# Performance work log

Measured on AMD Instinct MI355X. Metric: run time of the kernel, lower is better.

Reference implementation:

```python
import jax, jax.numpy as jnp
import numpy as np

NUM_GROUPS = 32
EPS = 1e-6


def group_norm(x, gamma, beta):
    # x: (b, c, h, w) -> normalize within 32 groups over (c/g, h, w)
    b, c, h, w = x.shape
    g = NUM_GROUPS
    xg = x.reshape(b, g, c // g, h, w)
    mean = xg.mean(axis=(2, 3, 4), keepdims=True)
    var = xg.var(axis=(2, 3, 4), keepdims=True)
    xg = (xg - mean) * jax.lax.rsqrt(var + EPS)
    xn = xg.reshape(b, c, h, w)
    return xn * gamma[None, :, None, None] + beta[None, :, None, None]


def setup_inputs() -> dict:
    key = jax.random.key(0)
    ks = jax.random.split(key, 4)
    b, c, h, w = 4, 512, 64, 64
    x = jax.random.normal(ks[0], (b, c, h, w), dtype=jnp.float32)
    gamma = jnp.ones((c,), dtype=jnp.float32)
    beta = jnp.zeros((c,), dtype=jnp.float32)
    w_qkv = jax.random.normal(ks[1], (3 * c, c), dtype=jnp.float32) * (1.0 / np.sqrt(c))
    b_qkv = jnp.zeros((3 * c,), dtype=jnp.float32)
    # NOTE: original init zeroes proj weight; use small random weights so the
    # attention path contributes to output/gradients in the baseline.
    w_proj = jax.random.normal(ks[2], (c, c), dtype=jnp.float32) * 0.02
    b_proj = jnp.zeros((c,), dtype=jnp.float32)
    return {"x": x, "gamma": gamma, "beta": beta, "w_qkv": w_qkv,
            "b_qkv": b_qkv, "w_proj": w_proj, "b_proj": b_proj}


def reference(x, gamma, beta, w_qkv, b_qkv, w_proj, b_proj):
    b, c, h, w = x.shape
    scale = c ** (-0.25)
    identity = x
    xn = group_norm(x, gamma, beta)
    # 1x1 conv == channel matmul: (b,c,h,w) x (3c,c) -> (b,3c,h,w)
    qkv = jnp.einsum('bchw,oc->bohw', xn, w_qkv) + b_qkv[None, :, None, None]
    qkv = qkv.reshape(b, 3 * c, h * w)
    q, k, v = jnp.split(qkv, 3, axis=1)          # each (b, c, N)
    attn = jnp.einsum('bci,bcj->bij', q * scale, k * scale)  # (b, N, N)
    attn = jax.nn.softmax(attn, axis=-1)
    out = jnp.einsum('bij,bcj->bci', attn, v)    # (b, c, N)
    out = out.reshape(b, c, h, w)
    out = jnp.einsum('bchw,oc->bohw', out, w_proj) + b_proj[None, :, None, None]
    return out + identity
```

## Files before the change

kernel.cpp:

```cpp
#include <hip/hip_runtime.h>
#include <hip/hip_fp8.h>
#include <stdint.h>

typedef unsigned short u16;
typedef unsigned char u8;
typedef __bf16 bf16x8 __attribute__((ext_vector_type(8)));
typedef float f32x4 __attribute__((ext_vector_type(4)));

__device__ __forceinline__ u16 f2bf(float f) {
  union { float f; unsigned u; } v; v.f = f;
  return (u16)((v.u + 0x7FFFu + ((v.u >> 16) & 1u)) >> 16);
}
__device__ __forceinline__ u8 f2f8(float f) {
  __hip_fp8_e4m3 h(f);
  return (u8)h.__x;
}

__device__ __forceinline__ void gld_lds16(const void* g, void* l) {
  uint32_t lo = (uint32_t)(uintptr_t)l;
  lo = __builtin_amdgcn_readfirstlane(lo);
  auto* lp = (__attribute__((address_space(3))) uint32_t*)(uintptr_t)lo;
  auto* gp = (const __attribute__((address_space(1))) uint32_t*)(uintptr_t)g;
  __builtin_amdgcn_global_load_lds(gp, lp, 16, 0, 0);
}

__global__ __launch_bounds__(256) void cvt_weights(
    const float* __restrict__ wq, const float* __restrict__ wp,
    u16* __restrict__ oq, u16* __restrict__ op) {
  int i = blockIdx.x * 256 + threadIdx.x;
  if (i < 1536 * 512) oq[i] = f2bf(wq[i]);
  if (i < 512 * 512)  op[i] = f2bf(wp[i]);
}

__global__ __launch_bounds__(256) void gn_stats(const float* __restrict__ x,
                                                float* __restrict__ stats) {
  int bg = blockIdx.x;
  const float* p = x + (size_t)bg * 65536;
  float s = 0.f, sq = 0.f;
  for (int i = threadIdx.x * 4; i < 65536; i += 1024) {
    float4 v = *(const float4*)(p + i);
    s += v.x + v.y + v.z + v.w;
    sq += v.x * v.x + v.y * v.y + v.z * v.z + v.w * v.w;
  }
  int lane = threadIdx.x & 63, w = threadIdx.x >> 6;
  for (int off = 32; off; off >>= 1) {
    s += __shfl_down(s, off);
    sq += __shfl_down(sq, off);
  }
  __shared__ float ls[4], lq[4];
  if (lane == 0) { ls[w] = s; lq[w] = sq; }
  __syncthreads();
  if (threadIdx.x == 0) {
    float S = ls[0] + ls[1] + ls[2] + ls[3];
    float Q = lq[0] + lq[1] + lq[2] + lq[3];
    float mean = S * (1.f / 65536.f);
    float var = Q * (1.f / 65536.f) - mean * mean;
    stats[bg * 2] = mean;
    stats[bg * 2 + 1] = rsqrtf(var + 1e-6f);
  }
}

__global__ __launch_bounds__(256) void gn_norm_t(const float* __restrict__ x,
    const float* __restrict__ stats, const float* __restrict__ gamma,
    const float* __restrict__ beta, u16* __restrict__ xnT) {
  __shared__ u16 tile[64][72];
  int b = blockIdx.z;
  int c0 = blockIdx.y * 64, n0 = blockIdx.x * 64;
  int t = threadIdx.x;
  int cl = t >> 2, ng = (t & 3) * 16;
  int c = c0 + cl;
  float mean = stats[(b * 32 + (c >> 4)) * 2];
  float rstd = stats[(b * 32 + (c >> 4)) * 2 + 1];
  float a = gamma[c] * rstd;
  float b2 = beta[c] - mean * a;
  const float* src = x + ((size_t)b * 512 + c) * 4096 + n0 + ng;
  u16 e[16];
  #pragma unroll
  for (int q = 0; q < 4; ++q) {
    float4 v = *(const float4*)(src + q * 4);
    e[q * 4 + 0] = f2bf(v.x * a + b2);
    e[q * 4 + 1] = f2bf(v.y * a + b2);
    e[q * 4 + 2] = f2bf(v.z * a + b2);
    e[q * 4 + 3] = f2bf(v.w * a + b2);
  }
  #pragma unroll
  for (int j = 0; j < 16; ++j) tile[ng + j][cl] = e[j];
  __syncthreads();
  int nl = t >> 2, cg = (t & 3) * 16;
  uint4 w0 = *(const uint4*)&tile[nl][cg];
  uint4 w1 = *(const uint4*)&tile[nl][cg + 8];
  u16* dst = xnT + ((size_t)b * 4096 + n0 + nl) * 512 + c0 + cg;
  *(uint4*)dst = w0;
  *(uint4*)(dst + 8) = w1;
}

template<int EPI>
__global__ __launch_bounds__(256) void gemm_nt(
    const u16* __restrict__ A, const u16* __restrict__ B,
    int lda, int ldb, int K,
    const float* __restrict__ bias, const float* __restrict__ resid,
    float scale, float* __restrict__ outF, void* __restrict__ outBv, int ldo,
    size_t azs, size_t bzs, size_t ozs) {
  __shared__ __align__(16) u16 smem[16384];
  const size_t z = blockIdx.z;
  A += z * azs; B += z * bzs;
  const int t = threadIdx.x;
  const int wave = t >> 6, lane = t & 63;
  const int wm = wave >> 1, wn = wave & 1;
  const int quad = lane >> 4, li = lane & 15;
  const int m0 = blockIdx.y * 128, n0 = blockIdx.x * 128;

  const int srow = lane >> 2;
  const int scol = (lane & 3) * 8;
  const u16* gA[2];
  const u16* gB[2];
  int ldsOff[2];
  #pragma unroll
  for (int r = 0; r < 2; ++r) {
    int rb = wave + 4 * r;
    gA[r] = A + (size_t)(m0 + rb * 16 + srow) * lda + scol;
    gB[r] = B + (size_t)(n0 + rb * 16 + srow) * ldb + scol;
    ldsOff[r] = rb * 512;
  }

  f32x4 zero = {0.f, 0.f, 0.f, 0.f};
  f32x4 acc[4][4];
  #pragma unroll
  for (int i = 0; i < 4; ++i)
    #pragma unroll
    for (int j = 0; j < 4; ++j) acc[i][j] = zero;

  #pragma unroll
  for (int r = 0; r < 2; ++r) {
    gld_lds16(gA[r], &smem[ldsOff[r]]);
    gld_lds16(gB[r], &smem[8192 + ldsOff[r]]);
  }
  __syncthreads();

  for (int kt = 0; kt < K; kt += 32) {
    const int s = (kt >> 5) & 1;
    if (kt + 32 < K) {
      const int ns = s ^ 1;
      #pragma unroll
      for (int r = 0; r < 2; ++r) {
        gld_lds16(gA[r] + kt + 32, &smem[ns * 4096 + ldsOff[r]]);
        gld_lds16(gB[r] + kt + 32, &smem[8192 + ns * 4096 + ldsOff[r]]);
      }
    }
    bf16x8 af[4], bf[4];
    #pragma unroll
    for (int i = 0; i < 4; ++i) {
      af[i] = *(const bf16x8*)&smem[s * 4096 +
               (wm * 64 + i * 16 + li) * 32 + quad * 8];
      bf[i] = *(const bf16x8*)&smem[8192 + s * 4096 +
               (wn * 64 + i * 16 + li) * 32 + quad * 8];
    }
    #pragma unroll
    for (int i = 0; i < 4; ++i)
      #pragma unroll
      for (int j = 0; j < 4; ++j)
        acc[i][j] = __builtin_amdgcn_mfma_f32_16x16x32_bf16(
            af[i], bf[j], acc[i][j], 0, 0, 0);
    __syncthreads();
  }

  if (EPI == 3) {
    outF += z * ozs; resid += z * ozs;
    #pragma unroll
    for (int i = 0; i < 4; ++i)
      #pragma unroll
      for (int j = 0; j < 4; ++j) {
        int mB = m0 + wm * 64 + i * 16 + quad * 4;
        int n = n0 + wn * 64 + j * 16 + li;
        #pragma unroll
        for (int r = 0; r < 4; ++r) {
          int m = mB + r;
          float v = acc[i][j][r] + bias[m] + resid[(size_t)m * ldo + n];
          outF[(size_t)m * ldo + n] = v;
        }
      }
    return;
  }

  u8* out8 = (u8*)outBv + z * ozs;
  u8* bnc = (u8*)smem;
  #pragma unroll
  for (int i = 0; i < 4; ++i) {
    int lm = wm * 64 + i * 16 + quad * 4;
    #pragma unroll
    for (int j = 0; j < 4; ++j) {
      int ln = wn * 64 + j * 16 + li;
      #pragma unroll
      for (int r = 0; r < 4; ++r) {
        float v = acc[i][j][r];
        u8 o;
        if (EPI == 4) o = f2f8((v + bias[n0 + ln]) * scale);
        else          o = f2f8(v + bias[m0 + lm + r]);
        bnc[(lm + r) * 144 + ln] = o;
      }
    }
  }
  __syncthreads();
  {
    int row = t >> 1, half = t & 1;
    const u8* src = &bnc[row * 144 + half * 64];
    u8* dst = out8 + (size_t)(m0 + row) * ldo + n0 + half * 64;
    #pragma unroll
    for (int cc = 0; cc < 4; ++cc)
      *(uint4*)(dst + cc * 16) = *(const uint4*)(src + cc * 16);
  }
}

template<int EPI, int SWZ>
__global__ __launch_bounds__(256) void gemm_nt8(
    const u8* __restrict__ A, const u8* __restrict__ B,
    int lda, int ldb, int K,
    const float* __restrict__ rsum, float* __restrict__ outF,
    void* __restrict__ outBv, int ldo,
    size_t azs, size_t bzs, size_t ozs) {
  __shared__ __align__(16) u8 smem[(EPI == 6) ? 34816 : 18432];
  const size_t z = blockIdx.z;
  A += z * azs; B += z * bzs;
  int bx = blockIdx.x, by = blockIdx.y;
  if (SWZ) {
    int lin = by * 32 + bx;
    int tt = lin >> 8, w = lin & 255;
    by = (tt >> 1) * 16 + (w >> 4);
    bx = (tt & 1) * 16 + (w & 15);
  }
  const int t = threadIdx.x;
  const int wave = t >> 6, lane = t & 63;
  const int wm = wave >> 1, wn = wave & 1;
  const int quad = lane >> 4, li = lane & 15;
  const int m0 = by * 128, n0 = bx * 128;

  const int srow = lane >> 1;
  const int scol = (lane & 1) * 16;
  const u8* gA = A + (size_t)(m0 + wave * 32 + srow) * lda + scol;
  const u8* gB = B + (size_t)(n0 + wave * 32 + srow) * ldb + scol;
  const int ldsOff = wave * 1024;

  f32x4 zero = {0.f, 0.f, 0.f, 0.f};
  f32x4 acc[4][4];
  #pragma unroll
  for (int i = 0; i < 4; ++i)
    #pragma unroll
    for (int j = 0; j < 4; ++j) acc[i][j] = zero;

  gld_lds16(gA, &smem[ldsOff]);
  gld_lds16(gB, &smem[8192 + ldsOff]);
  __syncthreads();

  for (int kt = 0; kt < K; kt += 32) {
    const int s = (kt >> 5) & 1;
    if (kt + 32 < K) {
      const int ns = s ^ 1;
      gld_lds16(gA + kt + 32, &smem[ns * 4096 + ldsOff]);
      gld_lds16(gB + kt + 32, &smem[8192 + ns * 4096 + ldsOff]);
    }
    long af[4], bf[4];
    #pragma unroll
    for (int i = 0; i < 4; ++i) {
      af[i] = *(const long*)&smem[s * 4096 +
               (wm * 64 + i * 16 + li) * 32 + quad * 8];
      bf[i] = *(const long*)&smem[8192 + s * 4096 +
               (wn * 64 + i * 16 + li) * 32 + quad * 8];
    }
    #pragma unroll
    for (int i = 0; i < 4; ++i)
      #pragma unroll
      for (int j = 0; j < 4; ++j)
        acc[i][j] = __builtin_amdgcn_mfma_f32_16x16x32_fp8_fp8(
            af[i], bf[j], acc[i][j], 0, 0, 0);
    __syncthreads();
  }

  if (EPI == 7) {
    float* rsF = outF + z * 4096;
    u8* outE = (u8*)outBv + z * ozs;
    #pragma unroll
    for (int i = 0; i < 4; ++i) {
      int lm = wm * 64 + i * 16 + quad * 4;
      float rs[4] = {0.f, 0.f, 0.f, 0.f};
      #pragma unroll
      for (int j = 0; j < 4; ++j) {
        int ln = wn * 64 + j * 16 + li;
        #pragma unroll
        for (int r = 0; r < 4; ++r) {
          float e = fminf(__expf(acc[i][j][r]), 448.f);
          smem[(lm + r) * 144 + ln] = f2f8(e);
          rs[r] += e;
        }
      }
      #pragma unroll
      for (int r = 0; r < 4; ++r) {
        rs[r] += __shfl_xor(rs[r], 1);
        rs[r] += __shfl_xor(rs[r], 2);
        rs[r] += __shfl_xor(rs[r], 4);
        rs[r] += __shfl_xor(rs[r], 8);
      }
      if (li == 0) {
        #pragma unroll
        for (int r = 0; r < 4; ++r) atomicAdd(&rsF[m0 + lm + r], rs[r]);
      }
    }
    __syncthreads();
    int row = t >> 1, half = t & 1;
    const u8* src = &smem[row * 144 + half * 64];
    u8* dst = outE + (size_t)(m0 + row) * ldo + n0 + half * 64;
    #pragma unroll
    for (int cc = 0; cc < 4; ++cc)
      *(uint4*)(dst + cc * 16) = *(const uint4*)(src + cc * 16);
  } else {
    const float* rsF = rsum + z * 4096;
    u16* outp = (u16*)outBv + z * ozs;
    u16* b16 = (u16*)smem;
    #pragma unroll
    for (int i = 0; i < 4; ++i) {
      int lm = wm * 64 + i * 16 + quad * 4;
      float rinv[4];
      #pragma unroll
      for (int r = 0; r < 4; ++r)
        rinv[r] = __builtin_amdgcn_rcpf(rsF[m0 + lm + r]);
      #pragma unroll
      for (int j = 0; j < 4; ++j) {
        int ln = wn * 64 + j * 16 + li;
        #pragma unroll
        for (int r = 0; r < 4; ++r)
          b16[(lm + r) * 136 + ln] = f2bf(acc[i][j][r] * rinv[r]);
      }
    }
    __syncthreads();
    int row = t >> 1, half = t & 1;
    const u16* src = &b16[row * 136 + half * 64];
    u16* dst = outp + (size_t)(m0 + row) * ldo + n0 + half * 64;
    #pragma unroll
    for (int cc = 0; cc < 8; ++cc)
      *(uint4*)(dst + cc * 8) = *(const uint4*)(src + cc * 8);
  }
}

extern "C" void kernel_launch(void* const* d_in, const int* in_sizes, int n_in,
                              void* d_out, int out_size, void* d_ws, size_t ws_size,
                              hipStream_t stream) {
  (void)in_sizes; (void)n_in; (void)out_size; (void)ws_size;
  const float* x      = (const float*)d_in[0];
  const float* gamma  = (const float*)d_in[1];
  const float* beta   = (const float*)d_in[2];
  const float* w_qkv  = (const float*)d_in[3];
  const float* b_qkv  = (const float*)d_in[4];
  const float* w_proj = (const float*)d_in[5];
  const float* b_proj = (const float*)d_in[6];
  float* out = (float*)d_out;

  const int C = 512, N = 4096;
  const size_t NC = (size_t)N * C;
  const float scale = 0.21022410381342863f;

  char* ws = (char*)d_ws;
  size_t off = 0;
  auto alloc = [&](size_t bytes) -> char* {
    char* p = ws + off; off += (bytes + 255) & ~(size_t)255; return p;
  };
  u16*   wq_bf  = (u16*)alloc((size_t)1536 * 512 * 2);
  u16*   wp_bf  = (u16*)alloc((size_t)512 * 512 * 2);
  float* stats  = (float*)alloc(128 * 2 * 4);
  float* rowsum = (float*)alloc((size_t)4 * N * 4);
  u16*   xnT    = (u16*)alloc((size_t)4 * NC * 2);
  u8*    qkT    = (u8*)alloc((size_t)4 * N * 1024);
  u8*    vbf    = (u8*)alloc((size_t)4 * 512 * 4096);
  u16*   ao     = (u16*)alloc((size_t)4 * NC * 2);
  u8*    E      = (u8*)alloc((size_t)4 * N * N);

  cvt_weights<<<3072, 256, 0, stream>>>(w_qkv, w_proj, wq_bf, wp_bf);
  gn_stats<<<128, 256, 0, stream>>>(x, stats);
  gn_norm_t<<<dim3(64, 8, 4), 256, 0, stream>>>(x, stats, gamma, beta, xnT);
  hipMemsetAsync(rowsum, 0, (size_t)4 * N * 4, stream);

  gemm_nt<4><<<dim3(8, 32, 4), 256, 0, stream>>>(
      xnT, wq_bf, 512, 512, 512, b_qkv, nullptr, scale,
      nullptr, qkT, 1024, NC, 0, (size_t)N * 1024);
  gemm_nt<5><<<dim3(32, 4, 4), 256, 0, stream>>>(
      wq_bf + (size_t)1024 * 512, xnT, 512, 512, 512, b_qkv + 1024, nullptr,
      0.f, nullptr, vbf, 4096, 0, NC, (size_t)512 * 4096);
  gemm_nt8<7, 1><<<dim3(32, 32, 4), 256, 0, stream>>>(
      qkT, qkT + 512, 1024, 1024, 512, nullptr, rowsum,
      E, 4096, (size_t)N * 1024, (size_t)N * 1024, (size_t)N * N);
  gemm_nt8<6, 0><<<dim3(4, 32, 4), 256, 0, stream>>>(
      E, vbf, 4096, 4096, 4096, rowsum, nullptr,
      ao, 512, (size_t)N * N, (size_t)512 * 4096, NC);
  gemm_nt<3><<<dim3(32, 4, 4), 256, 0, stream>>>(
      wp_bf, ao, 512, 512, 512, b_proj, x, 0.f,
      out, nullptr, 4096, 0, NC, NC);
}
```

Before: 405.8 us.

## Replace QK^T fp8 GEMM with a 256x256-tile triple-buffered pipelined kernel

Adds a dedicated QK^T scores kernel that uses 256x256 output tiles with 8 waves, a three-stage LDS ring filled by global_load_lds, and MFMA phases interleaved with partial prefetches, barriers and s_setprio. It also remaps block indices for locality across batches. It keeps the exp/clamp/fp8 store and atomic row-sum epilogue. The aim is more data reuse per tile and load latency hidden behind MFMA work, at the cost of a 96KB LDS footprint and more register pressure, which can limit occupancy.

```diff
diff --git a/kernel.cpp b/kernel.cpp
--- a/kernel.cpp
+++ b/kernel.cpp
@@ -275,43 +275,7 @@
     __syncthreads();
   }
 
-  if (EPI == 7) {
-    float* rsF = outF + z * 4096;
-    u8* outE = (u8*)outBv + z * ozs;
-    #pragma unroll
-    for (int i = 0; i < 4; ++i) {
-      int lm = wm * 64 + i * 16 + quad * 4;
-      float rs[4] = {0.f, 0.f, 0.f, 0.f};
-      #pragma unroll
-      for (int j = 0; j < 4; ++j) {
-        int ln = wn * 64 + j * 16 + li;
-        #pragma unroll
-        for (int r = 0; r < 4; ++r) {
-          float e = fminf(__expf(acc[i][j][r]), 448.f);
-          smem[(lm + r) * 144 + ln] = f2f8(e);
-          rs[r] += e;
-        }
-      }
-      #pragma unroll
-      for (int r = 0; r < 4; ++r) {
-        rs[r] += __shfl_xor(rs[r], 1);
-        rs[r] += __shfl_xor(rs[r], 2);
-        rs[r] += __shfl_xor(rs[r], 4);
-        rs[r] += __shfl_xor(rs[r], 8);
-      }
-      if (li == 0) {
-        #pragma unroll
-        for (int r = 0; r < 4; ++r) atomicAdd(&rsF[m0 + lm + r], rs[r]);
-      }
-    }
-    __syncthreads();
-    int row = t >> 1, half = t & 1;
-    const u8* src = &smem[row * 144 + half * 64];
-    u8* dst = outE + (size_t)(m0 + row) * ldo + n0 + half * 64;
-    #pragma unroll
-    for (int cc = 0; cc < 4; ++cc)
-      *(uint4*)(dst + cc * 16) = *(const uint4*)(src + cc * 16);
-  } else {
+  {
     const float* rsF = rsum + z * 4096;
     u16* outp = (u16*)outBv + z * ozs;
     u16* b16 = (u16*)smem;
@@ -337,6 +301,196 @@
     #pragma unroll
     for (int cc = 0; cc < 8; ++cc)
       *(uint4*)(dst + cc * 8) = *(const uint4*)(src + cc * 8);
+  }
+}
+
+__global__ __launch_bounds__(512, 2) void qk8p(
+    const u8* __restrict__ A, const u8* __restrict__ B,
+    float* __restrict__ rowsum, u8* __restrict__ outE) {
+  __shared__ __align__(16) u8 smem[98304];
+
+  int gblk = (blockIdx.z * 16 + blockIdx.y) * 16 + blockIdx.x;
+  int work = (gblk & 7) * 128 + (gblk >> 3);
+  int z  = work >> 8;
+  int wr = work & 255;
+  int by = wr >> 4, bx = wr & 15;
+  const int m0 = by * 256, n0 = bx * 256;
+  A += (size_t)z * 4096 * 1024;
+  B += (size_t)z * 4096 * 1024;
+  float* rsF = rowsum + (size_t)z * 4096;
+  u8* outp = outE + (size_t)z * 4096 * 4096;
+
+  const int t = threadIdx.x;
+  const int lane = t & 63, w = t >> 6;
+  const int wm = w >> 2, wn = w & 3;
+  const int quad = lane >> 4, li = lane & 15;
+
+  const u8* gA[2];
+  const u8* gB[2];
+  uint32_t lA[2], lB[2];
+  #pragma unroll
+  for (int g = 0; g < 2; ++g) {
+    int row = t >> 1, c = t & 1;
+    gA[g] = A + (size_t)(m0 + row) * 1024 + g * 32 + c * 16;
+    gB[g] = B + (size_t)(n0 + row) * 1024 + g * 32 + c * 16;
+    lA[g] = g * 8192 + w * 1024;
+    lB[g] = 16384 + g * 8192 + w * 1024;
+  }
+
+  const int lo = li * 32 + quad * 8;
+  const uint32_t aB0 = (uint32_t)wm * 4096;
+  const uint32_t bB0 = 16384 + (uint32_t)wn * 2048;
+
+  f32x4 zero = {0.f, 0.f, 0.f, 0.f};
+  f32x4 acc[8][4];
+  #pragma unroll
+  for (int i = 0; i < 8; ++i)
+    #pragma unroll
+    for (int j = 0; j < 4; ++j) acc[i][j] = zero;
+
+  #pragma unroll
+  for (int tt = 0; tt < 2; ++tt) {
+    gld_lds16(gA[0] + tt * 64, &smem[tt * 32768 + lA[0]]);
+    gld_lds16(gB[0] + tt * 64, &smem[tt * 32768 + lB[0]]);
+    gld_lds16(gA[1] + tt * 64, &smem[tt * 32768 + lA[1]]);
+    gld_lds16(gB[1] + tt * 64, &smem[tt * 32768 + lB[1]]);
+  }
+  asm volatile("s_waitcnt vmcnt(4)" ::: "memory");
+  asm volatile("s_barrier" ::: "memory");
+
+  uint32_t bo = 0, bp = 65536;
+  #pragma unroll 1
+  for (int tt = 0; tt < 8; ++tt) {
+    const bool pf = tt < 6;
+    const int kp = tt * 64 + 128;
+    long a[8], b0[4], b1[4];
+
+    #pragma unroll
+    for (int i = 0; i < 4; ++i)
+      #pragma unroll
+      for (int k = 0; k < 2; ++k)
+        a[i * 2 + k] = *(const long*)&smem[bo + k * 8192 + aB0 + i * 512 + lo];
+    #pragma unroll
+    for (int j = 0; j < 2; ++j)
+      #pragma unroll
+      for (int k = 0; k < 2; ++k)
+        b0[j * 2 + k] = *(const long*)&smem[bo + k * 8192 + bB0 + j * 512 + lo];
+    if (pf) gld_lds16(gA[0] + kp, &smem[bp + lA[0]]);
+    asm volatile("s_barrier" ::: "memory");
+    __builtin_amdgcn_s_setprio(1);
+    #pragma unroll
+    for (int i = 0; i < 4; ++i)
+      #pragma unroll
+      for (int j = 0; j < 2; ++j) {
+        acc[i][j] = __builtin_amdgcn_mfma_f32_16x16x32_fp8_fp8(
+            a[i * 2 + 0], b0[j * 2 + 0], acc[i][j], 0, 0, 0);
+        acc[i][j] = __builtin_amdgcn_mfma_f32_16x16x32_fp8_fp8(
+            a[i * 2 + 1], b0[j * 2 + 1], acc[i][j], 0, 0, 0);
+      }
+    __builtin_amdgcn_s_setprio(0);
+    asm volatile("s_barrier" ::: "memory");
+
+    #pragma unroll
+    for (int j = 0; j < 2; ++j)
+      #pragma unroll
+      for (int k = 0; k < 2; ++k)
+        b1[j * 2 + k] =
+            *(const long*)&smem[bo + k * 8192 + bB0 + 1024 + j * 512 + lo];
+    if (pf) gld_lds16(gB[0] + kp, &smem[bp + lB[0]]);
+    asm volatile("s_barrier" ::: "memory");
+    __builtin_amdgcn_s_setprio(1);
+    #pragma unroll
+    for (int i = 0; i < 4; ++i)
+      #pragma unroll
+      for (int j = 0; j < 2; ++j) {
+        acc[i][2 + j] = __builtin_amdgcn_mfma_f32_16x16x32_fp8_fp8(
+            a[i * 2 + 0], b1[j * 2 + 0], acc[i][2 + j], 0, 0, 0);
+        acc[i][2 + j] = __builtin_amdgcn_mfma_f32_16x16x32_fp8_fp8(
+            a[i * 2 + 1], b1[j * 2 + 1], acc[i][2 + j], 0, 0, 0);
+      }
+    __builtin_amdgcn_s_setprio(0);
+    asm volatile("s_barrier" ::: "memory");
+
+    #pragma unroll
+    for (int i = 0; i < 4; ++i)
+      #pragma unroll
+      for (int k = 0; k < 2; ++k)
+        a[i * 2 + k] =
+            *(const long*)&smem[bo + k * 8192 + aB0 + 2048 + i * 512 + lo];
+    if (pf) gld_lds16(gA[1] + kp, &smem[bp + lA[1]]);
+    asm volatile("s_barrier" ::: "memory");
+    __builtin_amdgcn_s_setprio(1);
+    #pragma unroll
+    for (int i = 0; i < 4; ++i)
+      #pragma unroll
+      for (int j = 0; j < 2; ++j) {
+        acc[4 + i][2 + j] = __builtin_amdgcn_mfma_f32_16x16x32_fp8_fp8(
+            a[i * 2 + 0], b1[j * 2 + 0], acc[4 + i][2 + j], 0, 0, 0);
+        acc[4 + i][2 + j] = __builtin_amdgcn_mfma_f32_16x16x32_fp8_fp8(
+            a[i * 2 + 1], b1[j * 2 + 1], acc[4 + i][2 + j], 0, 0, 0);
+      }
+    __builtin_amdgcn_s_setprio(0);
+    asm volatile("s_barrier" ::: "memory");
+
+    if (pf) {
+      gld_lds16(gB[1] + kp, &smem[bp + lB[1]]);
+      asm volatile("s_waitcnt vmcnt(4)" ::: "memory");
+    } else {
+      asm volatile("s_waitcnt vmcnt(0)" ::: "memory");
+    }
+    asm volatile("s_barrier" ::: "memory");
+    __builtin_amdgcn_s_setprio(1);
+    #pragma unroll
+    for (int i = 0; i < 4; ++i)
+      #pragma unroll
+      for (int j = 0; j < 2; ++j) {
+        acc[4 + i][j] = __builtin_amdgcn_mfma_f32_16x16x32_fp8_fp8(
+            a[i * 2 + 0], b0[j * 2 + 0], acc[4 + i][j], 0, 0, 0);
+        acc[4 + i][j] = __builtin_amdgcn_mfma_f32_16x16x32_fp8_fp8(
+            a[i * 2 + 1], b0[j * 2 + 1], acc[4 + i][j], 0, 0, 0);
+      }
+    __builtin_amdgcn_s_setprio(0);
+    asm volatile("s_barrier" ::: "memory");
+
+    bo += 32768; if (bo == 98304) bo = 0;
+    bp += 32768; if (bp == 98304) bp = 0;
+  }
+
+  u8* bnc = smem;
+  #pragma unroll
+  for (int I = 0; I < 8; ++I) {
+    int lm = wm * 128 + I * 16 + quad * 4;
+    float rs[4] = {0.f, 0.f, 0.f, 0.f};
+    #pragma unroll
+    for (int j = 0; j < 4; ++j) {
+      int ln = wn * 64 + j * 16 + li;
+      #pragma unroll
+      for (int r = 0; r < 4; ++r) {
+        float e = fminf(__expf(acc[I][j][r]), 448.f);
+        bnc[(lm + r) * 272 + ln] = f2f8(e);
+        rs[r] += e;
+      }
+    }
+    #pragma unroll
+    for (int r = 0; r < 4; ++r) {
+      rs[r] += __shfl_xor(rs[r], 1);
+      rs[r] += __shfl_xor(rs[r], 2);
+      rs[r] += __shfl_xor(rs[r], 4);
+      rs[r] += __shfl_xor(rs[r], 8);
+    }
+    if (li == 0) {
+      #pragma unroll
+      for (int r = 0; r < 4; ++r) atomicAdd(&rsF[m0 + lm + r], rs[r]);
+    }
+  }
+  __syncthreads();
+  {
+    int row = t >> 1, half = t & 1;
+    const u8* src = &bnc[row * 272 + half * 128];
+    u8* dst = outp + (size_t)(m0 + row) * 4096 + n0 + half * 128;
+    #pragma unroll
+    for (int cc = 0; cc < 8; ++cc)
+      *(uint4*)(dst + cc * 16) = *(const uint4*)(src + cc * 16);
   }
 }
 
@@ -383,9 +537,7 @@
   gemm_nt<5><<<dim3(32, 4, 4), 256, 0, stream>>>(
       wq_bf + (size_t)1024 * 512, xnT, 512, 512, 512, b_qkv + 1024, nullptr,
       0.f, nullptr, vbf, 4096, 0, NC, (size_t)512 * 4096);
-  gemm_nt8<7, 1><<<dim3(32, 32, 4), 256, 0, stream>>>(
-      qkT, qkT + 512, 1024, 1024, 512, nullptr, rowsum,
-      E, 4096, (size_t)N * 1024, (size_t)N * 1024, (size_t)N * N);
+  qk8p<<<dim3(16, 16, 4), 512, 0, stream>>>(qkT, qkT + 512, rowsum, E);
   gemm_nt8<6, 0><<<dim3(4, 32, 4), 256, 0, stream>>>(
       E, vbf, 4096, 4096, 4096, rowsum, nullptr,
       ao, 512, (size_t)N * N, (size_t)512 * 4096, NC);
```

Result: slower. 444.6 us (+9.6%).

## Triple-buffer FP8 GEMM LDS loads with swizzled layout and partial vmcnt waits

Applied to the files above, without the earlier changes.

The FP8 NT GEMM mainloop moves from double to triple buffering in LDS. It prefetches two K-tiles ahead and replaces full __syncthreads with s_waitcnt vmcnt(2) plus s_barrier, so global loads stay in flight across iterations. It also XOR-swizzles the global-to-LDS row mapping and the matching LDS read offsets to cut bank conflicts on the fragment loads. LDS use grows from 18 KB to 24 KB per block for non-EPI6 variants, which may reduce occupancy.

```diff
diff --git a/kernel.cpp b/kernel.cpp
--- a/kernel.cpp
+++ b/kernel.cpp
@@ -218,7 +218,7 @@
     const float* __restrict__ rsum, float* __restrict__ outF,
     void* __restrict__ outBv, int ldo,
     size_t azs, size_t bzs, size_t ozs) {
-  __shared__ __align__(16) u8 smem[(EPI == 6) ? 34816 : 18432];
+  __shared__ __align__(16) u8 smem[(EPI == 6) ? 34816 : 24576];
   const size_t z = blockIdx.z;
   A += z * azs; B += z * bzs;
   int bx = blockIdx.x, by = blockIdx.y;
@@ -234,11 +234,22 @@
   const int quad = lane >> 4, li = lane & 15;
   const int m0 = by * 128, n0 = bx * 128;
 
-  const int srow = lane >> 1;
-  const int scol = (lane & 1) * 16;
-  const u8* gA = A + (size_t)(m0 + wave * 32 + srow) * lda + scol;
-  const u8* gB = B + (size_t)(n0 + wave * 32 + srow) * ldb + scol;
+  const int us = lane ^ ((lane >> 3) & 7);
+  const int srow = (us >> 1) & 31;
+  const int shalf = us & 1;
+  const u8* gA = A + (size_t)(m0 + wave * 32 + srow) * lda + shalf * 16;
+  const u8* gB = B + (size_t)(n0 + wave * 32 + srow) * ldb + shalf * 16;
   const int ldsOff = wave * 1024;
+
+  const int h = quad >> 1, qlo = (quad & 1) * 8;
+  int aoff[4], boff[4];
+  #pragma unroll
+  for (int i = 0; i < 4; ++i) {
+    int r5 = (i & 1) * 16 + li;
+    int p = (2 * r5 + h) ^ ((r5 >> 2) & 7);
+    aoff[i] = (wm * 2 + (i >> 1)) * 1024 + p * 16 + qlo;
+    boff[i] = (wn * 2 + (i >> 1)) * 1024 + p * 16 + qlo;
+  }
 
   f32x4 zero = {0.f, 0.f, 0.f, 0.f};
   f32x4 acc[4][4];
@@ -248,23 +259,25 @@
     for (int j = 0; j < 4; ++j) acc[i][j] = zero;
 
   gld_lds16(gA, &smem[ldsOff]);
-  gld_lds16(gB, &smem[8192 + ldsOff]);
-  __syncthreads();
-
+  gld_lds16(gB, &smem[12288 + ldsOff]);
+  gld_lds16(gA + 32, &smem[4096 + ldsOff]);
+  gld_lds16(gB + 32, &smem[12288 + 4096 + ldsOff]);
+  asm volatile("s_waitcnt vmcnt(2)" ::: "memory");
+  asm volatile("s_barrier" ::: "memory");
+
+  int s = 0;
   for (int kt = 0; kt < K; kt += 32) {
-    const int s = (kt >> 5) & 1;
-    if (kt + 32 < K) {
-      const int ns = s ^ 1;
-      gld_lds16(gA + kt + 32, &smem[ns * 4096 + ldsOff]);
-      gld_lds16(gB + kt + 32, &smem[8192 + ns * 4096 + ldsOff]);
-    }
+    if (kt + 64 < K) {
+      const int ns = (s == 0) ? 2 : s - 1;
+      gld_lds16(gA + kt + 64, &smem[ns * 4096 + ldsOff]);
+      gld_lds16(gB + kt + 64, &smem[12288 + ns * 4096 + ldsOff]);
+    }
+    const int sb = s * 4096;
     long af[4], bf[4];
     #pragma unroll
     for (int i = 0; i < 4; ++i) {
-      af[i] = *(const long*)&smem[s * 4096 +
-               (wm * 64 + i * 16 + li) * 32 + quad * 8];
-      bf[i] = *(const long*)&smem[8192 + s * 4096 +
-               (wn * 64 + i * 16 + li) * 32 + quad * 8];
+      af[i] = *(const long*)&smem[sb + aoff[i]];
+      bf[i] = *(const long*)&smem[12288 + sb + boff[i]];
     }
     #pragma unroll
     for (int i = 0; i < 4; ++i)
@@ -272,8 +285,14 @@
       for (int j = 0; j < 4; ++j)
         acc[i][j] = __builtin_amdgcn_mfma_f32_16x16x32_fp8_fp8(
             af[i], bf[j], acc[i][j], 0, 0, 0);
-    __syncthreads();
-  }
+    if (kt + 32 < K) {
+      if (kt + 64 < K) asm volatile("s_waitcnt vmcnt(2)" ::: "memory");
+      else             asm volatile("s_waitcnt vmcnt(0)" ::: "memory");
+      asm volatile("s_barrier" ::: "memory");
+    }
+    s = (s == 2) ? 0 : s + 1;
+  }
+  __syncthreads();
 
   if (EPI == 7) {
     float* rsF = outF + z * 4096;
```

Measured after the change: 386.0 us. -4.9%, faster.
